# Kernel optimization log

Hardware: AMD Instinct MI355X
Metric: run time of the kernel (lower is better)

The kernel has to match this reference:

```python
import jax, jax.numpy as jnp
import numpy as np

B, H, W, N, DX, DZ = 4, 64, 64, 4096, 2, 128
INIT_LS = 0.1


def setup_inputs() -> dict:
    key = jax.random.key(0)
    k1, k2, k3, k4 = jax.random.split(key, 4)
    xc_off_grid = jax.random.uniform(k1, (B, N, DX), dtype=jnp.float32)
    # regular grid coordinates in [0, 1]^2, broadcast over batch
    gy, gx = jnp.meshgrid(jnp.linspace(0.0, 1.0, H), jnp.linspace(0.0, 1.0, W), indexing="ij")
    xc_on_grid = jnp.broadcast_to(jnp.stack([gy, gx], axis=-1)[None], (B, H, W, DX)).astype(jnp.float32)
    zc_off_grid = jax.random.normal(k2, (B, N, DZ), dtype=jnp.float32)
    zc_on_grid = jax.random.normal(k3, (B, H, W, DZ), dtype=jnp.float32)
    # lengthscale_param = log(exp(init_lengthscale) - 1)  (inverse softplus)
    lengthscale_param = jnp.log(jnp.expm1(jnp.full((DX,), INIT_LS, dtype=jnp.float32)))
    return {
        "xc_off_grid": xc_off_grid,
        "xc_on_grid": xc_on_grid,
        "zc_off_grid": zc_off_grid,
        "zc_on_grid": zc_on_grid,
        "lengthscale_param": lengthscale_param,
        "ignore_on_grid": 0,
    }


def reference(xc_off_grid, xc_on_grid, zc_off_grid, zc_on_grid, lengthscale_param, ignore_on_grid):
    b = xc_on_grid.shape[0]
    grid_shape = xc_on_grid.shape[1:-1]
    dz = zc_off_grid.shape[-1]
    xg = xc_on_grid.reshape(b, -1, xc_on_grid.shape[-1])  # [b, m, dx]
    lengthscale = 1e-05 + jax.nn.softplus(lengthscale_param)  # [dx]
    # squared scaled distances: [b, m, n]
    diff = (xg[:, :, None, :] - xc_off_grid[:, None, :, :]) / lengthscale
    weights = jnp.exp(-0.5 * jnp.sum(diff * diff, axis=-1))  # [b, m, n]
    zc = jnp.einsum("bmn,bnd->bmd", weights, zc_off_grid)  # [b, m, dz]
    if not ignore_on_grid:
        zc = zc + zc_on_grid.reshape(b, -1, dz)
    return zc.reshape((b,) + grid_shape + (dz,))
```

## Files before the change

kernel.cpp:

```cpp
#include <hip/hip_runtime.h>

#define HH 64
#define WW 64
#define NN 4096
#define DZc 128
#define KS 8
#define BK 64
#define NKT (NN / KS / BK)
#define CELLS 2097152
#define WS_NEED (8ull * CELLS * 2ull)

typedef __fp16 v2fp16 __attribute__((ext_vector_type(2)));
typedef _Float16 v4h __attribute__((ext_vector_type(4)));
typedef _Float16 v8h __attribute__((ext_vector_type(8)));
typedef float v16f __attribute__((ext_vector_type(16)));

__device__ __forceinline__ unsigned pk16(float lo, float hi){
  union { v2fp16 h; unsigned u; } c;
  c.h = __builtin_amdgcn_cvt_pkrtz(lo, hi);
  return c.u;
}
__device__ __forceinline__ float fexp2(float x){ return __builtin_amdgcn_exp2f(x); }

__global__ void init_out_kernel(const float4* __restrict__ zc_on,
                                const int* __restrict__ ignore,
                                float4* __restrict__ out){
  int i = blockIdx.x * blockDim.x + threadIdx.x;
  float4 v = zc_on[i];
  if (ignore[0]) { v.x = 0.f; v.y = 0.f; v.z = 0.f; v.w = 0.f; }
  out[i] = v;
}

__global__ void reduce_kernel(const v4h* __restrict__ part,
                              const float4* __restrict__ zc_on,
                              const int* __restrict__ ignore,
                              float4* __restrict__ out){
  int i = blockIdx.x * blockDim.x + threadIdx.x;
  float4 s = zc_on[i];
  if (ignore[0]) { s.x = 0.f; s.y = 0.f; s.z = 0.f; s.w = 0.f; }
  #pragma unroll
  for (int ks = 0; ks < KS; ++ks){
    v4h p = part[(size_t)ks * (CELLS / 4) + i];
    s.x += (float)p[0]; s.y += (float)p[1]; s.z += (float)p[2]; s.w += (float)p[3];
  }
  out[i] = s;
}

__global__ __launch_bounds__(256, 2)
void setconv_gemm_kernel(const float* __restrict__ xc_off,
                         const float* __restrict__ xc_on,
                         const float* __restrict__ zc_off,
                         const float* __restrict__ lsp,
                         _Float16* __restrict__ part,
                         float* __restrict__ out)
{
  __shared__ unsigned short zt[2][128][68];
  __shared__ unsigned short gt[2][40][72];

  const int tid = threadIdx.x;
  const int bid = blockIdx.x;
  const int ks  = bid >> 6;
  const int bm  = bid & 63;
  const int b   = bm >> 4;
  const int mt  = bm & 15;
  const int iy0 = (mt >> 3) * 32;
  const int ix0 = (mt & 7) * 8;
  const int nbase = ks * (NN / KS);

  const float lsy = 1e-5f + log1pf(expf(lsp[0]));
  const float lsx = 1e-5f + log1pf(expf(lsp[1]));
  const float LOG2E = 1.44269504088896340736f;
  const float ay = -0.5f * LOG2E / (lsy * lsy);
  const float ax = -0.5f * LOG2E / (lsx * lsx);

  const int gp = tid & 31;
  const int gr = tid >> 5;
  float gc[5], ga[5];
  #pragma unroll
  for (int i = 0; i < 5; ++i){
    int row = gr + 8 * i;
    if (row < 32){ gc[i] = xc_on[((b * HH + iy0 + row) * WW) * 2];        ga[i] = ay; }
    else         { gc[i] = xc_on[(b * HH * WW + ix0 + row - 32) * 2 + 1]; ga[i] = ax; }
  }

  const int zd  = (tid & 63) | (((tid >> 6) & 1) << 6);
  const int zkh = tid >> 7;

  const int lane = tid & 63;
  const int wv  = tid >> 6;
  const int l31 = lane & 31;
  const int lh  = lane >> 5;
  const int gxr = 32 + (l31 & 7);
  const int gyr = wv * 8 + (l31 >> 3);

  v16f acc[2][4];
  #pragma unroll
  for (int m = 0; m < 2; ++m)
    #pragma unroll
    for (int d = 0; d < 4; ++d)
      #pragma unroll
      for (int r = 0; r < 16; ++r)
        acc[m][d][r] = 0.f;

  const float* xb = xc_off + (size_t)b * NN * 2;
  const float* zb = zc_off + (size_t)b * NN * DZc;

  {
    const int n0 = nbase;
    float4 xq = *(const float4*)&xb[(size_t)(n0 + 2 * gp) * 2];
    unsigned* gw = (unsigned*)&gt[0][0][0];
    #pragma unroll
    for (int i = 0; i < 5; ++i){
      int row = gr + 8 * i;
      float s0 = (row < 32) ? xq.x : xq.y;
      float s1 = (row < 32) ? xq.z : xq.w;
      float d0 = gc[i] - s0, d1 = gc[i] - s1;
      gw[row * 36 + gp] = pk16(fexp2(ga[i] * d0 * d0), fexp2(ga[i] * d1 * d1));
    }
    float zv[32];
    #pragma unroll
    for (int i = 0; i < 32; ++i)
      zv[i] = zb[(size_t)(n0 + zkh * 32 + i) * DZc + zd];
    #pragma unroll
    for (int j = 0; j < 8; ++j){
      union { unsigned u[2]; double d; } w;
      w.u[0] = pk16(zv[4 * j],     zv[4 * j + 1]);
      w.u[1] = pk16(zv[4 * j + 2], zv[4 * j + 3]);
      *(double*)&zt[0][zd][zkh * 32 + 4 * j] = w.d;
    }
  }
  __syncthreads();

  #pragma unroll 1
  for (int kt = 0; kt < NKT; ++kt){
    const int buf  = kt & 1;
    const int nbuf = buf ^ 1;
    const bool have_next = (kt + 1 < NKT);
    const int n1 = nbase + (kt + 1) * BK;

    float zv[32];
    float4 xq_n = (float4){0.f, 0.f, 0.f, 0.f};
    if (have_next){
      #pragma unroll
      for (int i = 0; i < 32; ++i)
        zv[i] = zb[(size_t)(n1 + zkh * 32 + i) * DZc + zd];
      xq_n = *(const float4*)&xb[(size_t)(n1 + 2 * gp) * 2];
    }

    #pragma unroll
    for (int kstep = 0; kstep < 4; ++kstep){
      const int k0 = kstep * 16 + lh * 8;
      const v8h xu = *(const v8h*)&gt[buf][gxr][k0];
      v8h bfr[4];
      #pragma unroll
      for (int dtl = 0; dtl < 4; ++dtl){
        union { v4h h[2]; v8h v; } zu;
        zu.h[0] = *(const v4h*)&zt[buf][dtl * 32 + l31][k0];
        zu.h[1] = *(const v4h*)&zt[buf][dtl * 32 + l31][k0 + 4];
        bfr[dtl] = zu.v;
      }
      #pragma unroll
      for (int mtl = 0; mtl < 2; ++mtl){
        const v8h yu = *(const v8h*)&gt[buf][gyr + mtl * 4][k0];
        v8h av = yu * xu;
        #pragma unroll
        for (int dtl = 0; dtl < 4; ++dtl)
          acc[mtl][dtl] = __builtin_amdgcn_mfma_f32_32x32x16_f16(av, bfr[dtl], acc[mtl][dtl], 0, 0, 0);
      }
    }

    if (have_next){
      #pragma unroll
      for (int j = 0; j < 8; ++j){
        union { unsigned u[2]; double d; } w;
        w.u[0] = pk16(zv[4 * j],     zv[4 * j + 1]);
        w.u[1] = pk16(zv[4 * j + 2], zv[4 * j + 3]);
        *(double*)&zt[nbuf][zd][zkh * 32 + 4 * j] = w.d;
      }
      unsigned* gw = (unsigned*)&gt[nbuf][0][0];
      #pragma unroll
      for (int i = 0; i < 5; ++i){
        int row = gr + 8 * i;
        float s0 = (row < 32) ? xq_n.x : xq_n.y;
        float s1 = (row < 32) ? xq_n.z : xq_n.w;
        float d0 = gc[i] - s0, d1 = gc[i] - s1;
        gw[row * 36 + gp] = pk16(fexp2(ga[i] * d0 * d0), fexp2(ga[i] * d1 * d1));
      }
    }
    __syncthreads();
  }

  if (part){
    _Float16* pw = part + (size_t)ks * CELLS;
    #pragma unroll
    for (int mtl = 0; mtl < 2; ++mtl)
      #pragma unroll
      for (int dtl = 0; dtl < 4; ++dtl){
        const int d = dtl * 32 + l31;
        #pragma unroll
        for (int reg = 0; reg < 16; ++reg){
          const int row = (reg & 3) + 8 * (reg >> 2) + 4 * lh;
          const int m = wv * 64 + mtl * 32 + row;
          const int iy = iy0 + (m >> 3);
          const int ix = ix0 + (m & 7);
          pw[((b * HH + iy) * WW + ix) * DZc + d] = (_Float16)acc[mtl][dtl][reg];
        }
      }
  } else {
    #pragma unroll
    for (int mtl = 0; mtl < 2; ++mtl)
      #pragma unroll
      for (int dtl = 0; dtl < 4; ++dtl){
        const int d = dtl * 32 + l31;
        #pragma unroll
        for (int reg = 0; reg < 16; ++reg){
          const int row = (reg & 3) + 8 * (reg >> 2) + 4 * lh;
          const int m = wv * 64 + mtl * 32 + row;
          const int iy = iy0 + (m >> 3);
          const int ix = ix0 + (m & 7);
          unsafeAtomicAdd(&out[((b * HH + iy) * WW + ix) * DZc + d], acc[mtl][dtl][reg]);
        }
      }
  }
}

extern "C" void kernel_launch(void* const* d_in, const int* in_sizes, int n_in,
                              void* d_out, int out_size, void* d_ws, size_t ws_size,
                              hipStream_t stream){
  const float* xc_off = (const float*)d_in[0];
  const float* xc_on  = (const float*)d_in[1];
  const float* zc_off = (const float*)d_in[2];
  const float* zc_on  = (const float*)d_in[3];
  const float* lsp    = (const float*)d_in[4];
  const int*   ign    = (const int*)d_in[5];
  float* out = (float*)d_out;

  if (ws_size >= WS_NEED){
    _Float16* part = (_Float16*)d_ws;
    setconv_gemm_kernel<<<KS * 64, 256, 0, stream>>>(xc_off, xc_on, zc_off, lsp, part, out);
    reduce_kernel<<<CELLS / 4 / 256, 256, 0, stream>>>((const v4h*)part, (const float4*)zc_on, ign, (float4*)out);
  } else {
    init_out_kernel<<<out_size / 1024, 256, 0, stream>>>((const float4*)zc_on, ign, (float4*)out);
    setconv_gemm_kernel<<<KS * 64, 256, 0, stream>>>(xc_off, xc_on, zc_off, lsp, nullptr, out);
  }
}
```

Measured before the change: 109.2 us.

## Prepack zc_off into transposed fp16 layout before the GEMM kernel

Adds a prepack kernel that converts zc_off to fp16 and transposes it to a [b][d][n] layout in workspace. The main GEMM kernel then loads 16-byte contiguous fp16 vectors per thread instead of 32 strided fp32 scalar loads with per-tile conversion. This cuts global load instructions and the register pressure of staging 32 floats. In exchange it adds an extra launch, a read and write pass over zc_off, and a larger workspace requirement.

```diff
diff --git a/kernel.cpp b/kernel.cpp
--- a/kernel.cpp
+++ b/kernel.cpp
@@ -8,12 +8,14 @@
 #define BK 64
 #define NKT (NN / KS / BK)
 #define CELLS 2097152
-#define WS_NEED (8ull * CELLS * 2ull)
+#define ZT_BYTES (4ull * 128 * 4096 * 2ull)
+#define WS_NEED (ZT_BYTES + 8ull * CELLS * 2ull)
 
 typedef __fp16 v2fp16 __attribute__((ext_vector_type(2)));
 typedef _Float16 v4h __attribute__((ext_vector_type(4)));
 typedef _Float16 v8h __attribute__((ext_vector_type(8)));
 typedef float v16f __attribute__((ext_vector_type(16)));
+typedef double v2d __attribute__((ext_vector_type(2)));
 
 __device__ __forceinline__ unsigned pk16(float lo, float hi){
   union { v2fp16 h; unsigned u; } c;
@@ -31,6 +33,45 @@
   out[i] = v;
 }
 
+__global__ __launch_bounds__(256, 4)
+void prepack_kernel(const float* __restrict__ zc_off, _Float16* __restrict__ zt_g){
+  __shared__ unsigned tt[128 * 34];
+  const int bidx = blockIdx.x;
+  const int b  = bidx >> 6;
+  const int n0 = (bidx & 63) * 64;
+  const int t  = threadIdx.x;
+
+  const int np = t >> 3;
+  const int d0 = (t & 7) * 16;
+  const float* r0 = zc_off + ((size_t)(b * NN + n0 + 2 * np)) * DZc + d0;
+  float4 a[4], c[4];
+  #pragma unroll
+  for (int i = 0; i < 4; ++i){
+    a[i] = *(const float4*)&r0[4 * i];
+    c[i] = *(const float4*)&r0[DZc + 4 * i];
+  }
+  const float* af = (const float*)a;
+  const float* cf = (const float*)c;
+  #pragma unroll
+  for (int j = 0; j < 16; ++j)
+    tt[(d0 + j) * 34 + np] = pk16(af[j], cf[j]);
+
+  __syncthreads();
+
+  const int d  = t >> 1;
+  const int nh = t & 1;
+  const unsigned* rr = tt + d * 34 + nh * 16;
+  _Float16* w = zt_g + ((size_t)(b * DZc + d)) * NN + n0 + nh * 32;
+  double v[8];
+  #pragma unroll
+  for (int j = 0; j < 8; ++j) v[j] = *(const double*)&rr[2 * j];
+  #pragma unroll
+  for (int j = 0; j < 4; ++j){
+    v2d s; s[0] = v[2 * j]; s[1] = v[2 * j + 1];
+    *(v2d*)&w[8 * j] = s;
+  }
+}
+
 __global__ void reduce_kernel(const v4h* __restrict__ part,
                               const float4* __restrict__ zc_on,
                               const int* __restrict__ ignore,
@@ -46,10 +87,12 @@
   out[i] = s;
 }
 
+template<bool PRE>
 __global__ __launch_bounds__(256, 2)
 void setconv_gemm_kernel(const float* __restrict__ xc_off,
                          const float* __restrict__ xc_on,
                          const float* __restrict__ zc_off,
+                         const _Float16* __restrict__ zpack,
                          const float* __restrict__ lsp,
                          _Float16* __restrict__ part,
                          float* __restrict__ out)
@@ -85,6 +128,8 @@
 
   const int zd  = (tid & 63) | (((tid >> 6) & 1) << 6);
   const int zkh = tid >> 7;
+  const _Float16* ztg = PRE ? (zpack + ((size_t)(b * DZc + zd)) * NN + nbase + zkh * 32)
+                            : (const _Float16*)nullptr;
 
   const int lane = tid & 63;
   const int wv  = tid >> 6;
@@ -117,16 +162,26 @@
       float d0 = gc[i] - s0, d1 = gc[i] - s1;
       gw[row * 36 + gp] = pk16(fexp2(ga[i] * d0 * d0), fexp2(ga[i] * d1 * d1));
     }
-    float zv[32];
-    #pragma unroll
-    for (int i = 0; i < 32; ++i)
-      zv[i] = zb[(size_t)(n0 + zkh * 32 + i) * DZc + zd];
-    #pragma unroll
-    for (int j = 0; j < 8; ++j){
-      union { unsigned u[2]; double d; } w;
-      w.u[0] = pk16(zv[4 * j],     zv[4 * j + 1]);
-      w.u[1] = pk16(zv[4 * j + 2], zv[4 * j + 3]);
-      *(double*)&zt[0][zd][zkh * 32 + 4 * j] = w.d;
+    if (PRE){
+      #pragma unroll
+      for (int i = 0; i < 4; ++i){
+        union { v8h v; double d[2]; } u;
+        u.v = *(const v8h*)&ztg[8 * i];
+        *(double*)&zt[0][zd][zkh * 32 + 8 * i]     = u.d[0];
+        *(double*)&zt[0][zd][zkh * 32 + 8 * i + 4] = u.d[1];
+      }
+    } else {
+      float zv[32];
+      #pragma unroll
+      for (int i = 0; i < 32; ++i)
+        zv[i] = zb[(size_t)(n0 + zkh * 32 + i) * DZc + zd];
+      #pragma unroll
+      for (int j = 0; j < 8; ++j){
+        union { unsigned u[2]; double d; } w;
+        w.u[0] = pk16(zv[4 * j],     zv[4 * j + 1]);
+        w.u[1] = pk16(zv[4 * j + 2], zv[4 * j + 3]);
+        *(double*)&zt[0][zd][zkh * 32 + 4 * j] = w.d;
+      }
     }
   }
   __syncthreads();
@@ -138,12 +193,19 @@
     const bool have_next = (kt + 1 < NKT);
     const int n1 = nbase + (kt + 1) * BK;
 
+    v8h zrn[4];
     float zv[32];
     float4 xq_n = (float4){0.f, 0.f, 0.f, 0.f};
     if (have_next){
-      #pragma unroll
-      for (int i = 0; i < 32; ++i)
-        zv[i] = zb[(size_t)(n1 + zkh * 32 + i) * DZc + zd];
+      if (PRE){
+        #pragma unroll
+        for (int i = 0; i < 4; ++i)
+          zrn[i] = *(const v8h*)&ztg[(kt + 1) * BK + 8 * i];
+      } else {
+        #pragma unroll
+        for (int i = 0; i < 32; ++i)
+          zv[i] = zb[(size_t)(n1 + zkh * 32 + i) * DZc + zd];
+      }
       xq_n = *(const float4*)&xb[(size_t)(n1 + 2 * gp) * 2];
     }
 
@@ -170,12 +232,22 @@
     }
 
     if (have_next){
-      #pragma unroll
-      for (int j = 0; j < 8; ++j){
-        union { unsigned u[2]; double d; } w;
-        w.u[0] = pk16(zv[4 * j],     zv[4 * j + 1]);
-        w.u[1] = pk16(zv[4 * j + 2], zv[4 * j + 3]);
-        *(double*)&zt[nbuf][zd][zkh * 32 + 4 * j] = w.d;
+      if (PRE){
+        #pragma unroll
+        for (int i = 0; i < 4; ++i){
+          union { v8h v; double d[2]; } u;
+          u.v = zrn[i];
+          *(double*)&zt[nbuf][zd][zkh * 32 + 8 * i]     = u.d[0];
+          *(double*)&zt[nbuf][zd][zkh * 32 + 8 * i + 4] = u.d[1];
+        }
+      } else {
+        #pragma unroll
+        for (int j = 0; j < 8; ++j){
+          union { unsigned u[2]; double d; } w;
+          w.u[0] = pk16(zv[4 * j],     zv[4 * j + 1]);
+          w.u[1] = pk16(zv[4 * j + 2], zv[4 * j + 3]);
+          *(double*)&zt[nbuf][zd][zkh * 32 + 4 * j] = w.d;
+        }
       }
       unsigned* gw = (unsigned*)&gt[nbuf][0][0];
       #pragma unroll
@@ -236,11 +308,13 @@
   float* out = (float*)d_out;
 
   if (ws_size >= WS_NEED){
-    _Float16* part = (_Float16*)d_ws;
-    setconv_gemm_kernel<<<KS * 64, 256, 0, stream>>>(xc_off, xc_on, zc_off, lsp, part, out);
+    _Float16* zpack = (_Float16*)d_ws;
+    _Float16* part  = (_Float16*)((char*)d_ws + ZT_BYTES);
+    prepack_kernel<<<4 * 64, 256, 0, stream>>>(zc_off, zpack);
+    setconv_gemm_kernel<true><<<KS * 64, 256, 0, stream>>>(xc_off, xc_on, zc_off, zpack, lsp, part, out);
     reduce_kernel<<<CELLS / 4 / 256, 256, 0, stream>>>((const v4h*)part, (const float4*)zc_on, ign, (float4*)out);
   } else {
     init_out_kernel<<<out_size / 1024, 256, 0, stream>>>((const float4*)zc_on, ign, (float4*)out);
-    setconv_gemm_kernel<<<KS * 64, 256, 0, stream>>>(xc_off, xc_on, zc_off, lsp, nullptr, out);
-  }
-}
+    setconv_gemm_kernel<false><<<KS * 64, 256, 0, stream>>>(xc_off, xc_on, zc_off, nullptr, lsp, nullptr, out);
+  }
+}
```

Measured after the change: 109.7 us. About the same (+0.4%).
